# Performance work log

Hardware: AMD Instinct MI355X
Metric: run time of the kernel (lower is better)

The kernel has to match this reference:

```python
import jax, jax.numpy as jnp
import numpy as np

N_NODES = 50000
N_EDGES = 1600000
IN_FEATS = 64
EDGE_INFEAT = 32
HID_FEATS = 128
OUT_FEATS = 4


def setup_inputs() -> dict:
    key = jax.random.key(0)
    ks = jax.random.split(key, 8)
    h = jax.random.normal(ks[0], (N_NODES, IN_FEATS), dtype=jnp.float32)
    edge_feat = jax.random.normal(ks[1], (N_EDGES, EDGE_INFEAT), dtype=jnp.float32)
    src = jax.random.randint(ks[2], (N_EDGES,), 0, N_NODES, dtype=jnp.int32)
    dst = jax.random.randint(ks[3], (N_EDGES,), 0, N_NODES, dtype=jnp.int32)
    cat_dim = 2 * IN_FEATS + EDGE_INFEAT
    # Kaiming-ish scaled weights (nn.Linear default scale ~ 1/sqrt(fan_in))
    W1_w = jax.random.normal(ks[4], (cat_dim, HID_FEATS), dtype=jnp.float32) / np.sqrt(cat_dim)
    W1_b = jax.random.normal(ks[5], (HID_FEATS,), dtype=jnp.float32) * 0.01
    W2_w = jax.random.normal(ks[6], (HID_FEATS, OUT_FEATS), dtype=jnp.float32) / np.sqrt(HID_FEATS)
    W2_b = jax.random.normal(ks[7], (OUT_FEATS,), dtype=jnp.float32) * 0.01
    return {"h": h, "edge_feat": edge_feat, "src": src, "dst": dst,
            "W1_w": W1_w, "W1_b": W1_b, "W2_w": W2_w, "W2_b": W2_b}


def reference(h, edge_feat, src, dst, W1_w, W1_b, W2_w, W2_b):
    # Gather per-edge src/dst node features.  [E, in_feats]
    h_u = jnp.take(h, src, axis=0)
    h_v = jnp.take(h, dst, axis=0)
    # Avoid materializing the [E, 2*in+edge] concat: split the GEMM over the
    # three weight blocks (same math as cat -> Linear).
    Wu = W1_w[:IN_FEATS]            # [in_feats, hid]
    Wv = W1_w[IN_FEATS:2 * IN_FEATS]
    We = W1_w[2 * IN_FEATS:]        # [edge_infeat, hid]
    hid = h_u @ Wu + h_v @ Wv + edge_feat @ We + W1_b  # [E, hid]
    hid = jax.nn.relu(hid)
    return hid @ W2_w + W2_b  # [E, 4]
```

## Files before the change

kernel.cpp:

```cpp
#include <hip/hip_runtime.h>
#include <hip/hip_bf16.h>

#define N_NODES 50000
#define N_EDGES 1600000
#define IN_F 64
#define E_F 32
#define HID 128
#define OUT_F 4

typedef __attribute__((ext_vector_type(4))) float f32x4;
typedef __attribute__((ext_vector_type(8))) short short8;
typedef __attribute__((ext_vector_type(4))) int i32x4;

__device__ inline short f2bf(float f) {
  union { float f; unsigned u; } v; v.f = f;
  unsigned r = v.u + 0x7FFFu + ((v.u >> 16) & 1u);
  return (short)(r >> 16);
}
__device__ inline float bf2f(short s) {
  union { unsigned u; float f; } v; v.u = ((unsigned)(unsigned short)s) << 16;
  return v.f;
}

__global__ __launch_bounds__(256) void node_pre(const float* __restrict__ h,
                                                const float* __restrict__ W1,
                                                short* __restrict__ P) {
  const int tid  = threadIdx.x;
  const int o    = tid & 127;
  const int half = tid >> 7;
  const int j    = (o & 7) * 16 + (o >> 3);

  float wreg[64];
#pragma unroll
  for (int k = 0; k < 64; ++k) wreg[k] = W1[(half * 64 + k) * 128 + j];

  const int n0 = blockIdx.x * 49;
  const int n1 = min(n0 + 49, N_NODES);
  for (int n = n0; n < n1; ++n) {
    const float* __restrict__ hrow = h + (size_t)n * IN_F;
    float a0 = 0.f, a1 = 0.f, a2 = 0.f, a3 = 0.f;
#pragma unroll
    for (int k = 0; k < 64; k += 4) {
      a0 = fmaf(hrow[k    ], wreg[k    ], a0);
      a1 = fmaf(hrow[k + 1], wreg[k + 1], a1);
      a2 = fmaf(hrow[k + 2], wreg[k + 2], a2);
      a3 = fmaf(hrow[k + 3], wreg[k + 3], a3);
    }
    P[(size_t)n * 256 + half * 128 + o] = f2bf((a0 + a1) + (a2 + a3));
  }
}

#define TPW 8
__global__ __launch_bounds__(256) void edge_mlp(
    const float* __restrict__ ef, const int* __restrict__ src,
    const int* __restrict__ dst, const float* __restrict__ W1,
    const float* __restrict__ b1, const float* __restrict__ W2,
    const float* __restrict__ b2, const short* __restrict__ P,
    float* __restrict__ out) {
  const int tid  = threadIdx.x;
  const int lane = tid & 63;
  const int wid  = tid >> 6;
  const int col  = lane & 15;
  const int rowg = lane >> 4;

  short8 bfrag[8];
#pragma unroll
  for (int t = 0; t < 8; ++t) {
#pragma unroll
    for (int i = 0; i < 8; ++i) {
      const float f = W1[(2 * IN_F + rowg * 8 + i) * HID + t * 16 + col];
      bfrag[t][i] = f2bf(f);
    }
  }
  float b1r[8];
  f32x4 w2r[8];
#pragma unroll
  for (int t = 0; t < 8; ++t) {
    b1r[t] = b1[t * 16 + col];
    w2r[t] = ((const f32x4*)W2)[t * 16 + col];
  }
  const f32x4 b2r = *((const f32x4*)b2);

  const int tile0 = (blockIdx.x * 4 + wid) * TPW;

  for (int tt = 0; tt < TPW; ++tt) {
    const int e0    = (tile0 + tt) * 16;
    const int ebase = e0 + rowg * 4;

    const i32x4 se = __builtin_nontemporal_load((const i32x4*)(src + ebase));
    const i32x4 de = __builtin_nontemporal_load((const i32x4*)(dst + ebase));

    const f32x4* ea = (const f32x4*)(ef + (size_t)(e0 + col) * E_F + rowg * 8);
    const f32x4 a0 = __builtin_nontemporal_load(ea);
    const f32x4 a1 = __builtin_nontemporal_load(ea + 1);
    short8 af;
#pragma unroll
    for (int i = 0; i < 4; ++i) af[i] = f2bf(a0[i]);
#pragma unroll
    for (int i = 0; i < 4; ++i) af[4 + i] = f2bf(a1[i]);

    f32x4 acc[8];
#pragma unroll
    for (int t = 0; t < 8; ++t)
      acc[t] = __builtin_amdgcn_mfma_f32_16x16x32_bf16(
          af, bfrag[t], (f32x4){0.f, 0.f, 0.f, 0.f}, 0, 0, 0);

    const int sidx[4] = {se.x, se.y, se.z, se.w};
    const int didx[4] = {de.x, de.y, de.z, de.w};
    short8 lu[4], lv[4];
#pragma unroll
    for (int q = 0; q < 4; ++q) {
      lu[q] = *(const short8*)(P + (size_t)sidx[q] * 256 + col * 8);
      lv[q] = *(const short8*)(P + (size_t)didx[q] * 256 + 128 + col * 8);
    }
    f32x4 part[4] = {(f32x4){0,0,0,0}, (f32x4){0,0,0,0},
                     (f32x4){0,0,0,0}, (f32x4){0,0,0,0}};
#pragma unroll
    for (int q = 0; q < 4; ++q) {
#pragma unroll
      for (int t = 0; t < 8; ++t) {
        float hid = acc[t][q] + bf2f(lu[q][t]) + bf2f(lv[q][t]) + b1r[t];
        hid = fmaxf(hid, 0.f);
#pragma unroll
        for (int o = 0; o < 4; ++o)
          part[q][o] = fmaf(hid, w2r[t][o], part[q][o]);
      }
    }

#pragma unroll
    for (int q = 0; q < 4; ++q) {
#pragma unroll
      for (int o = 0; o < 4; ++o) {
        float v = part[q][o];
        v += __shfl_xor(v, 1);
        v += __shfl_xor(v, 2);
        v += __shfl_xor(v, 4);
        v += __shfl_xor(v, 8);
        part[q][o] = v + b2r[o];
      }
    }
    if (col == 0) {
#pragma unroll
      for (int q = 0; q < 4; ++q)
        __builtin_nontemporal_store(part[q], (f32x4*)out + ebase + q);
    }
  }
}

extern "C" void kernel_launch(void* const* d_in, const int* in_sizes, int n_in,
                              void* d_out, int out_size, void* d_ws, size_t ws_size,
                              hipStream_t stream) {
  const float* h   = (const float*)d_in[0];
  const float* ef  = (const float*)d_in[1];
  const int*   src = (const int*)d_in[2];
  const int*   dst = (const int*)d_in[3];
  const float* W1  = (const float*)d_in[4];
  const float* b1  = (const float*)d_in[5];
  const float* W2  = (const float*)d_in[6];
  const float* b2  = (const float*)d_in[7];
  float* out = (float*)d_out;
  short* P   = (short*)d_ws;

  hipLaunchKernelGGL(node_pre, dim3((N_NODES + 48) / 49), dim3(256), 0, stream,
                     h, W1, P);
  hipLaunchKernelGGL(edge_mlp, dim3(N_EDGES / (16 * 4 * TPW)), dim3(256), 0,
                     stream, ef, src, dst, W1, b1, W2, b2, P, out);
}
```

Before: 514.3 us.

## Software-pipeline edge tile loads and gathers across loop iterations

```diff
diff --git a/kernel.cpp b/kernel.cpp
--- a/kernel.cpp
+++ b/kernel.cpp
@@ -83,47 +83,62 @@
 
   const int tile0 = (blockIdx.x * 4 + wid) * TPW;
 
-  for (int tt = 0; tt < TPW; ++tt) {
-    const int e0    = (tile0 + tt) * 16;
-    const int ebase = e0 + rowg * 4;
+  i32x4 se[2], de[2];
+  f32x4 ea0[2], ea1[2];
+  short8 lu[2][4], lv[2][4];
 
-    const i32x4 se = __builtin_nontemporal_load((const i32x4*)(src + ebase));
-    const i32x4 de = __builtin_nontemporal_load((const i32x4*)(dst + ebase));
+  auto LOAD_IT = [&](int t, int p) {
+    const int e0 = (tile0 + t) * 16;
+    se[p] = __builtin_nontemporal_load((const i32x4*)(src + e0 + rowg * 4));
+    de[p] = __builtin_nontemporal_load((const i32x4*)(dst + e0 + rowg * 4));
+    const f32x4* ea = (const f32x4*)(ef + (size_t)(e0 + col) * E_F + rowg * 8);
+    ea0[p] = __builtin_nontemporal_load(ea);
+    ea1[p] = __builtin_nontemporal_load(ea + 1);
+  };
+  auto GATHER = [&](int p) {
+#pragma unroll
+    for (int q = 0; q < 4; ++q) {
+      lu[p][q] = *(const short8*)(P + (size_t)se[p][q] * 256 + col * 8);
+      lv[p][q] = *(const short8*)(P + (size_t)de[p][q] * 256 + 128 + col * 8);
+    }
+  };
 
-    const f32x4* ea = (const f32x4*)(ef + (size_t)(e0 + col) * E_F + rowg * 8);
-    const f32x4 a0 = __builtin_nontemporal_load(ea);
-    const f32x4 a1 = __builtin_nontemporal_load(ea + 1);
+  LOAD_IT(0, 0);
+  GATHER(0);
+  LOAD_IT(1, 1);
+
+#pragma unroll
+  for (int t = 0; t < TPW; ++t) {
+    const int p  = t & 1;
+    const int np = p ^ 1;
+    const int ebase = (tile0 + t) * 16 + rowg * 4;
+
+    if (t + 1 < TPW) GATHER(np);
+
     short8 af;
 #pragma unroll
-    for (int i = 0; i < 4; ++i) af[i] = f2bf(a0[i]);
+    for (int i = 0; i < 4; ++i) af[i] = f2bf(ea0[p][i]);
 #pragma unroll
-    for (int i = 0; i < 4; ++i) af[4 + i] = f2bf(a1[i]);
+    for (int i = 0; i < 4; ++i) af[4 + i] = f2bf(ea1[p][i]);
+    if (t + 2 < TPW) LOAD_IT(t + 2, p);
 
     f32x4 acc[8];
 #pragma unroll
-    for (int t = 0; t < 8; ++t)
-      acc[t] = __builtin_amdgcn_mfma_f32_16x16x32_bf16(
-          af, bfrag[t], (f32x4){0.f, 0.f, 0.f, 0.f}, 0, 0, 0);
+    for (int u = 0; u < 8; ++u)
+      acc[u] = __builtin_amdgcn_mfma_f32_16x16x32_bf16(
+          af, bfrag[u], (f32x4){0.f, 0.f, 0.f, 0.f}, 0, 0, 0);
 
-    const int sidx[4] = {se.x, se.y, se.z, se.w};
-    const int didx[4] = {de.x, de.y, de.z, de.w};
-    short8 lu[4], lv[4];
-#pragma unroll
-    for (int q = 0; q < 4; ++q) {
-      lu[q] = *(const short8*)(P + (size_t)sidx[q] * 256 + col * 8);
-      lv[q] = *(const short8*)(P + (size_t)didx[q] * 256 + 128 + col * 8);
-    }
     f32x4 part[4] = {(f32x4){0,0,0,0}, (f32x4){0,0,0,0},
                      (f32x4){0,0,0,0}, (f32x4){0,0,0,0}};
 #pragma unroll
     for (int q = 0; q < 4; ++q) {
 #pragma unroll
-      for (int t = 0; t < 8; ++t) {
-        float hid = acc[t][q] + bf2f(lu[q][t]) + bf2f(lv[q][t]) + b1r[t];
+      for (int u = 0; u < 8; ++u) {
+        float hid = acc[u][q] + bf2f(lu[p][q][u]) + bf2f(lv[p][q][u]) + b1r[u];
         hid = fmaxf(hid, 0.f);
 #pragma unroll
         for (int o = 0; o < 4; ++o)
-          part[q][o] = fmaf(hid, w2r[t][o], part[q][o]);
+          part[q][o] = fmaf(hid, w2r[u][o], part[q][o]);
       }
     }
 
```

Result: no change. 516.1 us (+0.4%).

## Gather bf16 node features per edge and fold all three GEMMs into MFMA

Applied to the files above, without the earlier changes.

```diff
diff --git a/kernel.cpp b/kernel.cpp
--- a/kernel.cpp
+++ b/kernel.cpp
@@ -10,68 +10,53 @@
 
 typedef __attribute__((ext_vector_type(4))) float f32x4;
 typedef __attribute__((ext_vector_type(8))) short short8;
-typedef __attribute__((ext_vector_type(4))) int i32x4;
 
 __device__ inline short f2bf(float f) {
   union { float f; unsigned u; } v; v.f = f;
   unsigned r = v.u + 0x7FFFu + ((v.u >> 16) & 1u);
   return (short)(r >> 16);
 }
-__device__ inline float bf2f(short s) {
-  union { unsigned u; float f; } v; v.u = ((unsigned)(unsigned short)s) << 16;
-  return v.f;
-}
 
-__global__ __launch_bounds__(256) void node_pre(const float* __restrict__ h,
-                                                const float* __restrict__ W1,
-                                                short* __restrict__ P) {
-  const int tid  = threadIdx.x;
-  const int o    = tid & 127;
-  const int half = tid >> 7;
-  const int j    = (o & 7) * 16 + (o >> 3);
-
-  float wreg[64];
+__global__ __launch_bounds__(256) void cast_h(const float* __restrict__ h,
+                                              short* __restrict__ h16) {
+  const int i = blockIdx.x * 256 + threadIdx.x;
+  if (i < N_NODES * IN_F / 8) {
+    const f32x4 a0 = ((const f32x4*)h)[i * 2];
+    const f32x4 a1 = ((const f32x4*)h)[i * 2 + 1];
+    short8 pk;
 #pragma unroll
-  for (int k = 0; k < 64; ++k) wreg[k] = W1[(half * 64 + k) * 128 + j];
-
-  const int n0 = blockIdx.x * 49;
-  const int n1 = min(n0 + 49, N_NODES);
-  for (int n = n0; n < n1; ++n) {
-    const float* __restrict__ hrow = h + (size_t)n * IN_F;
-    float a0 = 0.f, a1 = 0.f, a2 = 0.f, a3 = 0.f;
+    for (int k = 0; k < 4; ++k) pk[k] = f2bf(a0[k]);
 #pragma unroll
-    for (int k = 0; k < 64; k += 4) {
-      a0 = fmaf(hrow[k    ], wreg[k    ], a0);
-      a1 = fmaf(hrow[k + 1], wreg[k + 1], a1);
-      a2 = fmaf(hrow[k + 2], wreg[k + 2], a2);
-      a3 = fmaf(hrow[k + 3], wreg[k + 3], a3);
-    }
-    P[(size_t)n * 256 + half * 128 + o] = f2bf((a0 + a1) + (a2 + a3));
+    for (int k = 0; k < 4; ++k) pk[4 + k] = f2bf(a1[k]);
+    ((short8*)h16)[i] = pk;
   }
 }
 
-#define TPW 8
+#define TPW 25
 __global__ __launch_bounds__(256) void edge_mlp(
     const float* __restrict__ ef, const int* __restrict__ src,
     const int* __restrict__ dst, const float* __restrict__ W1,
     const float* __restrict__ b1, const float* __restrict__ W2,
-    const float* __restrict__ b2, const short* __restrict__ P,
+    const float* __restrict__ b2, const short* __restrict__ h16,
     float* __restrict__ out) {
+  __shared__ short8 Bl[5 * 8 * 64];
+
   const int tid  = threadIdx.x;
   const int lane = tid & 63;
   const int wid  = tid >> 6;
   const int col  = lane & 15;
   const int rowg = lane >> 4;
 
-  short8 bfrag[8];
+  for (int e = tid; e < 5 * 8 * 64; e += 256) {
+    const int ln = e & 63, t8 = (e >> 6) & 7, c = e >> 9;
+    const int kbase = c * 32 + (ln >> 4) * 8;
+    short8 w;
 #pragma unroll
-  for (int t = 0; t < 8; ++t) {
-#pragma unroll
-    for (int i = 0; i < 8; ++i) {
-      const float f = W1[(2 * IN_F + rowg * 8 + i) * HID + t * 16 + col];
-      bfrag[t][i] = f2bf(f);
-    }
+    for (int i = 0; i < 8; ++i)
+      w[i] = f2bf(W1[(kbase + i) * HID + t8 * 16 + (ln & 15)]);
+    Bl[e] = w;
   }
+
   float b1r[8];
   f32x4 w2r[8];
 #pragma unroll
@@ -80,46 +65,50 @@
     w2r[t] = ((const f32x4*)W2)[t * 16 + col];
   }
   const f32x4 b2r = *((const f32x4*)b2);
+  __syncthreads();
 
-  const int tile0 = (blockIdx.x * 4 + wid) * TPW;
+  const int g0 = (blockIdx.x * 4 + wid) * TPW;
 
   for (int tt = 0; tt < TPW; ++tt) {
-    const int e0    = (tile0 + tt) * 16;
-    const int ebase = e0 + rowg * 4;
+    const int e0 = (g0 + tt) * 16;
 
-    const i32x4 se = __builtin_nontemporal_load((const i32x4*)(src + ebase));
-    const i32x4 de = __builtin_nontemporal_load((const i32x4*)(dst + ebase));
-
+    const int sn = src[e0 + col];
+    const int dn = dst[e0 + col];
+    const short8 au0 = *(const short8*)(h16 + (size_t)sn * IN_F + rowg * 8);
+    const short8 au1 = *(const short8*)(h16 + (size_t)sn * IN_F + 32 + rowg * 8);
+    const short8 av0 = *(const short8*)(h16 + (size_t)dn * IN_F + rowg * 8);
+    const short8 av1 = *(const short8*)(h16 + (size_t)dn * IN_F + 32 + rowg * 8);
     const f32x4* ea = (const f32x4*)(ef + (size_t)(e0 + col) * E_F + rowg * 8);
     const f32x4 a0 = __builtin_nontemporal_load(ea);
     const f32x4 a1 = __builtin_nontemporal_load(ea + 1);
-    short8 af;
+    short8 ae;
 #pragma unroll
-    for (int i = 0; i < 4; ++i) af[i] = f2bf(a0[i]);
+    for (int i = 0; i < 4; ++i) ae[i] = f2bf(a0[i]);
 #pragma unroll
-    for (int i = 0; i < 4; ++i) af[4 + i] = f2bf(a1[i]);
+    for (int i = 0; i < 4; ++i) ae[4 + i] = f2bf(a1[i]);
 
     f32x4 acc[8];
 #pragma unroll
-    for (int t = 0; t < 8; ++t)
+    for (int t = 0; t < 8; ++t) {
+      f32x4 c4 = __builtin_amdgcn_mfma_f32_16x16x32_bf16(
+          au0, Bl[(0 * 8 + t) * 64 + lane], (f32x4){0.f, 0.f, 0.f, 0.f}, 0, 0, 0);
+      c4 = __builtin_amdgcn_mfma_f32_16x16x32_bf16(
+          au1, Bl[(1 * 8 + t) * 64 + lane], c4, 0, 0, 0);
+      c4 = __builtin_amdgcn_mfma_f32_16x16x32_bf16(
+          av0, Bl[(2 * 8 + t) * 64 + lane], c4, 0, 0, 0);
+      c4 = __builtin_amdgcn_mfma_f32_16x16x32_bf16(
+          av1, Bl[(3 * 8 + t) * 64 + lane], c4, 0, 0, 0);
       acc[t] = __builtin_amdgcn_mfma_f32_16x16x32_bf16(
-          af, bfrag[t], (f32x4){0.f, 0.f, 0.f, 0.f}, 0, 0, 0);
+          ae, Bl[(4 * 8 + t) * 64 + lane], c4, 0, 0, 0);
+    }
 
-    const int sidx[4] = {se.x, se.y, se.z, se.w};
-    const int didx[4] = {de.x, de.y, de.z, de.w};
-    short8 lu[4], lv[4];
-#pragma unroll
-    for (int q = 0; q < 4; ++q) {
-      lu[q] = *(const short8*)(P + (size_t)sidx[q] * 256 + col * 8);
-      lv[q] = *(const short8*)(P + (size_t)didx[q] * 256 + 128 + col * 8);
-    }
     f32x4 part[4] = {(f32x4){0,0,0,0}, (f32x4){0,0,0,0},
                      (f32x4){0,0,0,0}, (f32x4){0,0,0,0}};
 #pragma unroll
     for (int q = 0; q < 4; ++q) {
 #pragma unroll
       for (int t = 0; t < 8; ++t) {
-        float hid = acc[t][q] + bf2f(lu[q][t]) + bf2f(lv[q][t]) + b1r[t];
+        float hid = acc[t][q] + b1r[t];
         hid = fmaxf(hid, 0.f);
 #pragma unroll
         for (int o = 0; o < 4; ++o)
@@ -142,7 +131,8 @@
     if (col == 0) {
 #pragma unroll
       for (int q = 0; q < 4; ++q)
-        __builtin_nontemporal_store(part[q], (f32x4*)out + ebase + q);
+        __builtin_nontemporal_store(part[q],
+                                    (f32x4*)out + e0 + rowg * 4 + q);
     }
   }
 }
@@ -159,10 +149,10 @@
   const float* W2  = (const float*)d_in[6];
   const float* b2  = (const float*)d_in[7];
   float* out = (float*)d_out;
-  short* P   = (short*)d_ws;
+  short* h16 = (short*)d_ws;
 
-  hipLaunchKernelGGL(node_pre, dim3((N_NODES + 48) / 49), dim3(256), 0, stream,
-                     h, W1, P);
+  hipLaunchKernelGGL(cast_h, dim3((N_NODES * IN_F / 8 + 255) / 256), dim3(256),
+                     0, stream, h, h16);
   hipLaunchKernelGGL(edge_mlp, dim3(N_EDGES / (16 * 4 * TPW)), dim3(256), 0,
-                     stream, ef, src, dst, W1, b1, W2, b2, P, out);
+                     stream, ef, src, dst, W1, b1, W2, b2, h16, out);
 }
```

Measured after the change: 595.3 us. 15.7% more time.
